# Kernel tuning notes

Hardware: AMD Instinct MI355X
Metric: run time of the kernel (lower is better)

Reference implementation:

```python
import jax, jax.numpy as jnp
import numpy as np

N = 8192      # nodes
E = 262144    # edges per graph (avg degree 32)
D_IN = 256
HID = 64
HEADS = 2
NEG_SLOPE = 0.2  # PyG GATConv leaky_relu slope


def _self_loops(ei, n):
    loop = jnp.arange(n, dtype=ei.dtype)
    return jnp.concatenate([ei[0], loop]), jnp.concatenate([ei[1], loop])


def gat_conv(x, src, dst, W, att_src, att_dst, b, concat):
    # PyG GATConv: h=[N,H,C]; alpha=softmax_dst(leaky_relu(a_s[src]+a_d[dst]))
    n = x.shape[0]
    H, C = att_src.shape
    h = (x @ W).reshape(n, H, C)
    a_s = (h * att_src).sum(-1)           # [N,H]
    a_d = (h * att_dst).sum(-1)           # [N,H]
    e = jax.nn.leaky_relu(a_s[src] + a_d[dst], NEG_SLOPE)  # [Etot,H]
    e = e - jax.ops.segment_max(e, dst, num_segments=n)[dst]
    e = jnp.exp(e)
    denom = jax.ops.segment_sum(e, dst, num_segments=n)[dst] + 1e-16
    alpha = e / denom                     # edge softmax per target node
    msg = h[src] * alpha[:, :, None]      # [Etot,H,C]
    out = jax.ops.segment_sum(msg, dst, num_segments=n)  # [N,H,C]
    out = out.reshape(n, H * C) if concat else out.mean(axis=1)
    return out + b


def gcn_conv(x, src, dst, W, b):
    # PyG GCNConv: D^{-1/2}(A+I)D^{-1/2} X W + b (self loops already appended)
    n = x.shape[0]
    h = x @ W
    deg = jax.ops.segment_sum(jnp.ones_like(src, jnp.float32), dst, num_segments=n)
    dinv = jax.lax.rsqrt(jnp.maximum(deg, 1.0))
    norm = dinv[src] * dinv[dst]          # [Etot]
    return jax.ops.segment_sum(h[src] * norm[:, None], dst, num_segments=n) + b


def cross_attn(q_in, kv_in, Wq, bq, Wk, bk, Wv, bv, Wo, bo, num_heads):
    n, d = q_in.shape
    hd = d // num_heads
    q = (q_in @ Wq + bq).reshape(n, num_heads, hd)
    k = (kv_in @ Wk + bk).reshape(n, num_heads, hd)
    v = (kv_in @ Wv + bv).reshape(n, num_heads, hd)
    scores = jnp.einsum('qhd,khd->hqk', q, k) / np.sqrt(hd).astype(np.float32)
    attn = jax.nn.softmax(scores, axis=-1)                 # [H,N,N]
    out = jnp.einsum('hqk,khd->qhd', attn, v).reshape(n, d) @ Wo + bo
    weights = attn.mean(axis=0)[None]                      # [1,N,N] avg heads (torch default)
    return out, weights


def setup_inputs():
    key = jax.random.key(0)
    ks = jax.random.split(key, 24)
    w = lambda k, s: jax.random.normal(k, s, jnp.float32) * 0.05
    inp = {
        'x': jax.random.normal(ks[0], (N, D_IN), jnp.float32),
        'edge_index_tkg': jax.random.randint(ks[1], (2, E), 0, N, jnp.int64 if jax.config.jax_enable_x64 else jnp.int32),
        'edge_index_ekg': jax.random.randint(ks[2], (2, E), 0, N, jnp.int64 if jax.config.jax_enable_x64 else jnp.int32),
        # GAT layer 1: heads=2, concat=True
        'gat1_W': w(ks[3], (D_IN, HEADS * HID)),
        'gat1_att_src': w(ks[4], (HEADS, HID)),
        'gat1_att_dst': w(ks[5], (HEADS, HID)),
        'gat1_b': jnp.zeros((HEADS * HID,), jnp.float32),
        # GAT layer 2: heads=1, concat=False
        'gat2_W': w(ks[6], (HEADS * HID, HID)),
        'gat2_att_src': w(ks[7], (1, HID)),
        'gat2_att_dst': w(ks[8], (1, HID)),
        'gat2_b': jnp.zeros((HID,), jnp.float32),
        # GCN layers
        'gcn1_W': w(ks[9], (D_IN, HID)),
        'gcn1_b': jnp.zeros((HID,), jnp.float32),
        'gcn2_W': w(ks[10], (HID, HID)),
        'gcn2_b': jnp.zeros((HID,), jnp.float32),
        # cross attention (hidden=64, 2 heads)
        'Wq': w(ks[11], (HID, HID)), 'bq': jnp.zeros((HID,), jnp.float32),
        'Wk': w(ks[12], (HID, HID)), 'bk': jnp.zeros((HID,), jnp.float32),
        'Wv': w(ks[13], (HID, HID)), 'bv': jnp.zeros((HID,), jnp.float32),
        'Wo': w(ks[14], (HID, HID)), 'bo': jnp.zeros((HID,), jnp.float32),
        # MLP head
        'fc1_W': w(ks[15], (2 * HID, HID)), 'fc1_b': jnp.zeros((HID,), jnp.float32),
        'fc2_W': w(ks[16], (HID, 1)), 'fc2_b': jnp.zeros((1,), jnp.float32),
    }
    return inp


def reference(x, edge_index_tkg, edge_index_ekg,
              gat1_W, gat1_att_src, gat1_att_dst, gat1_b,
              gat2_W, gat2_att_src, gat2_att_dst, gat2_b,
              gcn1_W, gcn1_b, gcn2_W, gcn2_b,
              Wq, bq, Wk, bk, Wv, bv, Wo, bo,
              fc1_W, fc1_b, fc2_W, fc2_b):
    n = x.shape[0]
    src_t, dst_t = _self_loops(edge_index_tkg, n)
    src_e, dst_e = _self_loops(edge_index_ekg, n)

    h_tkg = jax.nn.elu(gat_conv(x, src_t, dst_t, gat1_W, gat1_att_src, gat1_att_dst, gat1_b, True))
    h_tkg = jax.nn.elu(gat_conv(h_tkg, src_t, dst_t, gat2_W, gat2_att_src, gat2_att_dst, gat2_b, False))

    h_ekg = jax.nn.relu(gcn_conv(x, src_e, dst_e, gcn1_W, gcn1_b))
    h_ekg = jax.nn.relu(gcn_conv(h_ekg, src_e, dst_e, gcn2_W, gcn2_b))

    h_attn, attn_weights = cross_attn(h_tkg, h_ekg, Wq, bq, Wk, bk, Wv, bv, Wo, bo, HEADS)

    h_fused = jnp.concatenate([h_tkg, h_attn], axis=1)   # [N, 2*HID]
    pred = (jax.nn.relu(h_fused @ fc1_W + fc1_b) @ fc2_W + fc2_b).squeeze(-1)
    return pred, attn_weights
```

## Files before the change

kernel.cpp:

```cpp
#include <hip/hip_runtime.h>
#include <cstdint>
#include <cstddef>

#define NN 8192
#define EE 262144
#define ET 270336

using short8  = __attribute__((ext_vector_type(8))) short;
using floatx4 = __attribute__((ext_vector_type(4))) float;

__device__ __forceinline__ unsigned short f2bf(float f) {
  unsigned int u = __float_as_uint(f);
  u += 0x7fffu + ((u >> 16) & 1u);
  return (unsigned short)(u >> 16);
}

__global__ void edge_hist2_k(const int* __restrict__ ei_t, const int* __restrict__ ei_e,
                             int* __restrict__ cnt_t, int* __restrict__ cnt_e) {
  int idx = blockIdx.x * 256 + threadIdx.x;
  int g = idx >= ET;
  int e = g ? idx - ET : idx;
  const int* ei = g ? ei_e : ei_t;
  int* cnt = g ? cnt_e : cnt_t;
  int d = (e < EE) ? ei[EE + e] : (e - EE);
  atomicAdd(&cnt[d], 1);
}

__global__ void scan2_k(int* cnt_t, int* off_t, int* cnt_e, int* off_e) {
  int* cnt = blockIdx.x ? cnt_e : cnt_t;
  int* off = blockIdx.x ? off_e : off_t;
  __shared__ int s[1024];
  int t = threadIdx.x;
  int v[8]; int base = t * 8; int sum = 0;
  #pragma unroll
  for (int j = 0; j < 8; ++j) { v[j] = cnt[base + j]; sum += v[j]; }
  s[t] = sum; __syncthreads();
  for (int o = 1; o < 1024; o <<= 1) {
    int x = (t >= o) ? s[t - o] : 0;
    __syncthreads();
    s[t] += x;
    __syncthreads();
  }
  int excl = s[t] - sum;
  #pragma unroll
  for (int j = 0; j < 8; ++j) { off[base + j] = excl; cnt[base + j] = excl; excl += v[j]; }
  if (t == 1023) off[NN] = excl;
}

__global__ void edge_scatter2_k(const int* __restrict__ ei_t, const int* __restrict__ ei_e,
                                int* __restrict__ pos_t, int* __restrict__ pos_e,
                                int* __restrict__ srcs_t, int* __restrict__ srcs_e) {
  int idx = blockIdx.x * 256 + threadIdx.x;
  int g = idx >= ET;
  int e = g ? idx - ET : idx;
  const int* ei = g ? ei_e : ei_t;
  int* pos = g ? pos_e : pos_t;
  int* srcs = g ? srcs_e : srcs_t;
  int sv, d;
  if (e < EE) { sv = ei[e]; d = ei[EE + e]; } else { sv = d = e - EE; }
  int p = atomicAdd(&pos[d], 1);
  srcs[p] = sv;
}

__device__ __forceinline__ void gemm_core(const float* __restrict__ A, int lda, int K,
                                          const float* __restrict__ Bs, int row0, int col,
                                          float acc[8]) {
  #pragma unroll
  for (int r = 0; r < 8; ++r) acc[r] = 0.f;
  for (int k = 0; k < K; k += 4) {
    float b0 = Bs[(k + 0) * 32 + col], b1 = Bs[(k + 1) * 32 + col];
    float b2 = Bs[(k + 2) * 32 + col], b3 = Bs[(k + 3) * 32 + col];
    #pragma unroll
    for (int r = 0; r < 8; ++r) {
      const float4 a4 = *(const float4*)(A + (size_t)(row0 + r) * lda + k);
      acc[r] = fmaf(a4.x, b0, acc[r]);
      acc[r] = fmaf(a4.y, b1, acc[r]);
      acc[r] = fmaf(a4.z, b2, acc[r]);
      acc[r] = fmaf(a4.w, b3, acc[r]);
    }
  }
}

__global__ __launch_bounds__(256) void mm_x_k(const float* __restrict__ x,
    const float* __restrict__ Wgat, const float* __restrict__ Wgcn,
    const float* __restrict__ as_w, const float* __restrict__ ad_w,
    float* __restrict__ h1, float* __restrict__ hg1,
    float* __restrict__ a_s1, float* __restrict__ a_d1) {
  __shared__ float Bs[256 * 32];
  const int tid = threadIdx.x, by = blockIdx.y;
  const bool gat = by < 4;
  const int NC = gat ? 128 : 64;
  const int c0 = gat ? by * 32 : (by - 4) * 32;
  const float* B = gat ? Wgat : Wgcn;
  for (int idx = tid; idx < 256 * 32; idx += 256)
    Bs[idx] = B[(idx >> 5) * NC + c0 + (idx & 31)];
  __syncthreads();
  const int row0 = blockIdx.x * 64 + (tid >> 5) * 8;
  const int col = tid & 31;
  float acc[8];
  gemm_core(x, 256, 256, Bs, row0, col, acc);
  if (gat) {
    #pragma unroll
    for (int r = 0; r < 8; ++r) h1[(size_t)(row0 + r) * 128 + c0 + col] = acc[r];
    const int head = c0 >> 6;
    const float asw = as_w[head * 64 + (c0 & 63) + col];
    const float adw = ad_w[head * 64 + (c0 & 63) + col];
    float ps[8], pd[8];
    #pragma unroll
    for (int r = 0; r < 8; ++r) { ps[r] = acc[r] * asw; pd[r] = acc[r] * adw; }
    #pragma unroll
    for (int m = 16; m >= 1; m >>= 1)
      #pragma unroll
      for (int r = 0; r < 8; ++r) { ps[r] += __shfl_xor(ps[r], m); pd[r] += __shfl_xor(pd[r], m); }
    if (col == 0) {
      #pragma unroll
      for (int r = 0; r < 8; ++r) {
        atomicAdd(&a_s1[(row0 + r) * 2 + head], ps[r]);
        atomicAdd(&a_d1[(row0 + r) * 2 + head], pd[r]);
      }
    }
  } else {
    #pragma unroll
    for (int r = 0; r < 8; ++r) hg1[(size_t)(row0 + r) * 64 + c0 + col] = acc[r];
  }
}

template<int H, int C>
__device__ __forceinline__ void gat_agg_body(const float* __restrict__ h,
    const float* __restrict__ a_s, const float* __restrict__ a_d,
    const int* __restrict__ off, const int* __restrict__ srcs,
    const float* __restrict__ bias, float* __restrict__ out, int ldout, int b) {
  constexpr int HC = H * C;
  const int tid = threadIdx.x;
  const int hd = tid / C;
  const int r0 = off[b], r1 = off[b + 1];
  __shared__ int s_src[HC];
  __shared__ float s_w[HC][H];
  float ad[H];
  #pragma unroll
  for (int hh = 0; hh < H; ++hh) ad[hh] = a_d[b * H + hh];
  float acc = 0.f, den = 0.f;
  for (int base = r0; base < r1; base += HC) {
    const int cnt = min(HC, r1 - base);
    const int cnt4 = (cnt + 3) & ~3;
    __syncthreads();
    int e = base + tid;
    if (e < r1) {
      int sv = srcs[e];
      s_src[tid] = sv;
      #pragma unroll
      for (int hh = 0; hh < H; ++hh) {
        float xv = a_s[sv * H + hh] + ad[hh];
        xv = xv > 0.f ? xv : 0.2f * xv;
        s_w[tid][hh] = __expf(xv);
      }
    } else if (tid < cnt4) {
      s_src[tid] = 0;
      #pragma unroll
      for (int hh = 0; hh < H; ++hh) s_w[tid][hh] = 0.f;
    }
    __syncthreads();
    for (int j = 0; j < cnt4; j += 4) {
      #pragma unroll
      for (int u = 0; u < 4; ++u) {
        float wv = s_w[j + u][hd];
        den += wv;
        acc = fmaf(wv, h[(size_t)s_src[j + u] * HC + tid], acc);
      }
    }
  }
  float o = acc / den + bias[tid];
  out[(size_t)b * ldout + tid] = o > 0.f ? o : (__expf(o) - 1.f);
}

template<int H, int C>
__global__ void gat_agg_k(const float* __restrict__ h, const float* __restrict__ a_s,
                          const float* __restrict__ a_d, const int* __restrict__ off,
                          const int* __restrict__ srcs, const float* __restrict__ bias,
                          float* __restrict__ out, int ldout) {
  gat_agg_body<H, C>(h, a_s, a_d, off, srcs, bias, out, ldout, blockIdx.x);
}

__global__ __launch_bounds__(128) void agg1_k(
    const float* __restrict__ h1, const float* __restrict__ a_s1, const float* __restrict__ a_d1,
    const int* __restrict__ off_t, const int* __restrict__ src_t,
    const float* __restrict__ gat1_b, float* __restrict__ g1out,
    const float* __restrict__ hg1, const int* __restrict__ off_e, const int* __restrict__ src_e,
    const float* __restrict__ gcn1_b, const float* __restrict__ gcn2_W, float* __restrict__ h2g) {
  const int tid = threadIdx.x;
  if (blockIdx.x < NN) {
    gat_agg_body<2, 64>(h1, a_s1, a_d1, off_t, src_t, gat1_b, g1out, 128, blockIdx.x);
  } else {
    const int nb = (blockIdx.x - NN) * 2;
    const int sub = tid >> 6, t = tid & 63;
    const int node = nb + sub;
    __shared__ int s_src2[2][64];
    __shared__ float s_nrm2[2][64];
    __shared__ float s_row2[2][64];
    const int r0 = off_e[node], r1 = off_e[node + 1];
    const int cA = off_e[nb + 1] - off_e[nb];
    const int cB = off_e[nb + 2] - off_e[nb + 1];
    const int trips = (max(cA, cB) + 63) >> 6;
    float dinv_b = rsqrtf((float)max(r1 - r0, 1));
    float acc = 0.f;
    for (int it = 0; it < trips; ++it) {
      const int cnt = min(64, r1 - (r0 + it * 64));
      const int cnt4 = (cnt + 3) & ~3;
      __syncthreads();
      int e = r0 + it * 64 + t;
      if (e < r1) {
        int sv = src_e[e];
        s_src2[sub][t] = sv;
        int ds = off_e[sv + 1] - off_e[sv];
        s_nrm2[sub][t] = dinv_b * rsqrtf((float)max(ds, 1));
      } else if (t < cnt4) {
        s_src2[sub][t] = 0;
        s_nrm2[sub][t] = 0.f;
      }
      __syncthreads();
      for (int j = 0; j < cnt4; j += 4) {
        #pragma unroll
        for (int u = 0; u < 4; ++u)
          acc = fmaf(s_nrm2[sub][j + u], hg1[(size_t)s_src2[sub][j + u] * 64 + t], acc);
      }
    }
    s_row2[sub][t] = fmaxf(acc + gcn1_b[t], 0.f);
    __syncthreads();
    float acc2 = 0.f;
    for (int k = 0; k < 64; ++k)
      acc2 = fmaf(s_row2[sub][k], gcn2_W[k * 64 + t], acc2);
    h2g[(size_t)node * 64 + t] = acc2;
  }
}

__global__ __launch_bounds__(256) void mm2_k(
    const float* __restrict__ g1out, const float* __restrict__ gat2_W,
    const float* __restrict__ gat2_as, const float* __restrict__ gat2_ad,
    float* __restrict__ h2, float* __restrict__ a_s2, float* __restrict__ a_d2,
    const float* __restrict__ h2g, const int* __restrict__ off_e, const int* __restrict__ src_e,
    const float* __restrict__ gcn2_b, float* __restrict__ hekg) {
  const int tid = threadIdx.x;
  if (blockIdx.x < 256) {
    __shared__ float Bs[128 * 32];
    const int bx = blockIdx.x & 127;
    const int c0 = (blockIdx.x >> 7) * 32;
    for (int idx = tid; idx < 128 * 32; idx += 256)
      Bs[idx] = gat2_W[(idx >> 5) * 64 + c0 + (idx & 31)];
    __syncthreads();
    const int row0 = bx * 64 + (tid >> 5) * 8;
    const int col = tid & 31;
    float acc[8];
    gemm_core(g1out, 128, 128, Bs, row0, col, acc);
    const float asw = gat2_as[c0 + col];
    const float adw = gat2_ad[c0 + col];
    float ps[8], pd[8];
    #pragma unroll
    for (int r = 0; r < 8; ++r) {
      h2[(size_t)(row0 + r) * 64 + c0 + col] = acc[r];
      ps[r] = acc[r] * asw; pd[r] = acc[r] * adw;
    }
    #pragma unroll
    for (int m = 16; m >= 1; m >>= 1)
      #pragma unroll
      for (int r = 0; r < 8; ++r) { ps[r] += __shfl_xor(ps[r], m); pd[r] += __shfl_xor(pd[r], m); }
    if (col == 0) {
      #pragma unroll
      for (int r = 0; r < 8; ++r) {
        atomicAdd(&a_s2[row0 + r], ps[r]);
        atomicAdd(&a_d2[row0 + r], pd[r]);
      }
    }
  } else {
    const int nb = (blockIdx.x - 256) * 4;
    const int sub = tid >> 6, t = tid & 63;
    const int node = nb + sub;
    __shared__ int s_src4[4][64];
    __shared__ float s_nrm4[4][64];
    const int r0 = off_e[node], r1 = off_e[node + 1];
    int cmax = 0;
    #pragma unroll
    for (int i = 0; i < 4; ++i) cmax = max(cmax, off_e[nb + i + 1] - off_e[nb + i]);
    const int trips = (cmax + 63) >> 6;
    float dinv_b = rsqrtf((float)max(r1 - r0, 1));
    float acc = 0.f;
    for (int it = 0; it < trips; ++it) {
      const int cnt = min(64, r1 - (r0 + it * 64));
      const int cnt4 = (cnt + 3) & ~3;
      __syncthreads();
      int e = r0 + it * 64 + t;
      if (e < r1) {
        int sv = src_e[e];
        s_src4[sub][t] = sv;
        int ds = off_e[sv + 1] - off_e[sv];
        s_nrm4[sub][t] = dinv_b * rsqrtf((float)max(ds, 1));
      } else if (t < cnt4) {
        s_src4[sub][t] = 0;
        s_nrm4[sub][t] = 0.f;
      }
      __syncthreads();
      for (int j = 0; j < cnt4; j += 4) {
        #pragma unroll
        for (int u = 0; u < 4; ++u)
          acc = fmaf(s_nrm4[sub][j + u], h2g[(size_t)s_src4[sub][j + u] * 64 + t], acc);
      }
    }
    hekg[(size_t)node * 64 + t] = fmaxf(acc + gcn2_b[t], 0.f);
  }
}

__global__ __launch_bounds__(256) void mm_qkv_k(const float* __restrict__ htkg,
    const float* __restrict__ hekg,
    const float* __restrict__ Wq, const float* __restrict__ bq,
    const float* __restrict__ Wk, const float* __restrict__ bk,
    const float* __restrict__ Wv, const float* __restrict__ bv,
    unsigned short* __restrict__ qb, unsigned short* __restrict__ kb,
    unsigned short* __restrict__ Vt) {
  __shared__ float Bs[64 * 32];
  __shared__ float Ts[32][65];
  const int tid = threadIdx.x, by = blockIdx.y;
  const int kind = by >> 1;
  const int c0 = (by & 1) * 32;
  const float* A = (kind == 0) ? htkg : hekg;
  const float* B = (kind == 0) ? Wq : (kind == 1) ? Wk : Wv;
  const float* bias = (kind == 0) ? bq : (kind == 1) ? bk : bv;
  for (int idx = tid; idx < 64 * 32; idx += 256)
    Bs[idx] = B[(idx >> 5) * 64 + c0 + (idx & 31)];
  __syncthreads();
  const int row0 = blockIdx.x * 64 + (tid >> 5) * 8;
  const int col = tid & 31;
  float acc[8];
  gemm_core(A, 64, 64, Bs, row0, col, acc);
  const float bb = bias[c0 + col];
  if (kind == 0) {
    const float SCL = 0.17677669529663687f * 1.4426950408889634f;
    #pragma unroll
    for (int r = 0; r < 8; ++r)
      qb[(size_t)(row0 + r) * 64 + c0 + col] = f2bf((acc[r] + bb) * SCL);
  } else if (kind == 1) {
    #pragma unroll
    for (int r = 0; r < 8; ++r)
      kb[(size_t)(row0 + r) * 64 + c0 + col] = f2bf(acc[r] + bb);
  } else {
    const int rl = (tid >> 5) * 8;
    #pragma unroll
    for (int r = 0; r < 8; ++r) Ts[col][rl + r] = acc[r] + bb;
    __syncthreads();
    const int c = tid >> 3, rr = (tid & 7) * 8;
    short8 pk;
    #pragma unroll
    for (int j = 0; j < 8; ++j) pk[j] = (short)f2bf(Ts[c][rr + j]);
    *(short8*)(Vt + (size_t)(c0 + c) * NN + blockIdx.x * 64 + rr) = pk;
  }
}

__global__ __launch_bounds__(512) void att_lsum_k(
    const unsigned short* __restrict__ qb, const unsigned short* __restrict__ kb,
    float* __restrict__ lsum) {
  __shared__ __align__(16) short Kbuf[2][64 * 64];
  const int tid = threadIdx.x;
  const int lane = tid & 63, wv = tid >> 6;
  const int ql = lane & 15, quad = lane >> 4;
  const int q0 = blockIdx.x * 128 + wv * 16;
  const int k0 = blockIdx.y * 1024;
  const floatx4 zf = {0.f, 0.f, 0.f, 0.f};

  short8 qf[2];
  #pragma unroll
  for (int h = 0; h < 2; ++h)
    qf[h] = *(const short8*)(qb + (size_t)(q0 + ql) * 64 + h * 32 + quad * 8);

  const int sr = tid >> 3, sc = tid & 7;
  const int swc = (sc ^ (sr & 7)) * 8;
  short8 krg;

  float lacc[2][4];
  #pragma unroll
  for (int h = 0; h < 2; ++h)
    #pragma unroll
    for (int r = 0; r < 4; ++r) lacc[h][r] = 0.f;

  {
    krg = *(const short8*)(kb + (size_t)(k0 + sr) * 64 + sc * 8);
    *(short8*)&Kbuf[0][sr * 64 + swc] = krg;
  }
  __syncthreads();

  for (int t = 0; t < 16; ++t) {
    if (t < 15)
      krg = *(const short8*)(kb + (size_t)(k0 + (t + 1) * 64 + sr) * 64 + sc * 8);
    const short* Kc = Kbuf[t & 1];
    #pragma unroll
    for (int kt = 0; kt < 4; ++kt) {
      const int row = kt * 16 + ql;
      short8 kf[2];
      #pragma unroll
      for (int h = 0; h < 2; ++h)
        kf[h] = *(const short8*)&Kc[row * 64 + ((h * 4 + quad) ^ (row & 7)) * 8];
      #pragma unroll
      for (int h = 0; h < 2; ++h) {
        floatx4 s = __builtin_amdgcn_mfma_f32_16x16x32_bf16(qf[h], kf[h], zf, 0, 0, 0);
        #pragma unroll
        for (int r = 0; r < 4; ++r) lacc[h][r] += __builtin_amdgcn_exp2f(s[r]);
      }
    }
    if (t < 15)
      *(short8*)&Kbuf[(t + 1) & 1][sr * 64 + swc] = krg;
    __syncthreads();
  }

  #pragma unroll
  for (int o = 8; o >= 1; o >>= 1)
    #pragma unroll
    for (int h = 0; h < 2; ++h)
      #pragma unroll
      for (int r = 0; r < 4; ++r)
        lacc[h][r] += __shfl_xor(lacc[h][r], o, 16);
  if (ql == 0) {
    #pragma unroll
    for (int h = 0; h < 2; ++h)
      #pragma unroll
      for (int r = 0; r < 4; ++r)
        atomicAdd(&lsum[(q0 + quad * 4 + r) * 2 + h], lacc[h][r]);
  }
}

__global__ __launch_bounds__(512, 4) void att_pv_k(
    const unsigned short* __restrict__ qb, const unsigned short* __restrict__ kb,
    const unsigned short* __restrict__ Vt, const float* __restrict__ lsum,
    float* __restrict__ attn, float* __restrict__ O) {
  __shared__ __align__(16) short Kbuf[2][64 * 64];
  __shared__ __align__(16) short Vbuf[2][64 * 64];
  __shared__ __align__(16) float Esh[8][2][16 * 36];
  const int tid = threadIdx.x;
  const int lane = tid & 63, wv = tid >> 6;
  const int ql = lane & 15, quad = lane >> 4;
  const int q0 = blockIdx.x * 128 + wv * 16;
  const int k0 = blockIdx.y * 1024;
  const floatx4 zf = {0.f, 0.f, 0.f, 0.f};

  short8 qf[2];
  #pragma unroll
  for (int h = 0; h < 2; ++h)
    qf[h] = *(const short8*)(qb + (size_t)(q0 + ql) * 64 + h * 32 + quad * 8);

  float invl[2][4];
  #pragma unroll
  for (int h = 0; h < 2; ++h)
    #pragma unroll
    for (int r = 0; r < 4; ++r)
      invl[h][r] = 1.0f / lsum[(q0 + quad * 4 + r) * 2 + h];

  const int sr = tid >> 3, sc = tid & 7;
  const int swc = (sc ^ (sr & 7)) * 8;
  short8 krg, vrg;

  floatx4 oacc[2][2];
  #pragma unroll
  for (int h = 0; h < 2; ++h)
    #pragma unroll
    for (int hf = 0; hf < 2; ++hf) oacc[h][hf] = zf;

  {
    krg = *(const short8*)(kb + (size_t)(k0 + sr) * 64 + sc * 8);
    vrg = *(const short8*)(Vt + (size_t)sr * NN + k0 + sc * 8);
    *(short8*)&Kbuf[0][sr * 64 + swc] = krg;
    *(short8*)&Vbuf[0][sr * 64 + swc] = vrg;
  }
  __syncthreads();

  for (int t = 0; t < 16; ++t) {
    if (t < 15) {
      krg = *(const short8*)(kb + (size_t)(k0 + (t + 1) * 64 + sr) * 64 + sc * 8);
      vrg = *(const short8*)(Vt + (size_t)sr * NN + k0 + (t + 1) * 64 + sc * 8);
    }
    const short* Kc = Kbuf[t & 1];
    const short* Vc = Vbuf[t & 1];
    #pragma unroll
    for (int ks = 0; ks < 2; ++ks) {
      short8 kf[2][2], vf[2][2];
      #pragma unroll
      for (int kt = 0; kt < 2; ++kt) {
        const int row = ks * 32 + kt * 16 + ql;
        #pragma unroll
        for (int h = 0; h < 2; ++h)
          kf[kt][h] = *(const short8*)&Kc[row * 64 + ((h * 4 + quad) ^ (row & 7)) * 8];
      }
      #pragma unroll
      for (int h = 0; h < 2; ++h)
        #pragma unroll
        for (int hf = 0; hf < 2; ++hf) {
          const int d = h * 32 + hf * 16 + ql;
          vf[h][hf] = *(const short8*)&Vc[d * 64 + ((ks * 4 + quad) ^ (d & 7)) * 8];
        }

      floatx4 p[2][2];
      #pragma unroll
      for (int h = 0; h < 2; ++h)
        #pragma unroll
        for (int kt = 0; kt < 2; ++kt) {
          floatx4 s = __builtin_amdgcn_mfma_f32_16x16x32_bf16(qf[h], kf[kt][h], zf, 0, 0, 0);
          #pragma unroll
          for (int r = 0; r < 4; ++r)
            p[h][kt][r] = __builtin_amdgcn_exp2f(s[r]) * invl[h][r];
        }
      #pragma unroll
      for (int kt = 0; kt < 2; ++kt)
        #pragma unroll
        for (int r = 0; r < 4; ++r)
          attn[(size_t)(q0 + quad * 4 + r) * NN + k0 + t * 64 + ks * 32 + kt * 16 + ql] =
              0.5f * (p[0][kt][r] + p[1][kt][r]);
      #pragma unroll
      for (int h = 0; h < 2; ++h)
        #pragma unroll
        for (int kt = 0; kt < 2; ++kt)
          #pragma unroll
          for (int r = 0; r < 4; ++r)
            Esh[wv][h][(quad * 4 + r) * 36 + kt * 16 + ql] = p[h][kt][r];
      #pragma unroll
      for (int h = 0; h < 2; ++h) {
        const float* ep = &Esh[wv][h][ql * 36 + quad * 8];
        float4 x0 = *(const float4*)ep;
        float4 x1 = *(const float4*)(ep + 4);
        short8 ef;
        ef[0] = (short)f2bf(x0.x); ef[1] = (short)f2bf(x0.y);
        ef[2] = (short)f2bf(x0.z); ef[3] = (short)f2bf(x0.w);
        ef[4] = (short)f2bf(x1.x); ef[5] = (short)f2bf(x1.y);
        ef[6] = (short)f2bf(x1.z); ef[7] = (short)f2bf(x1.w);
        #pragma unroll
        for (int hf = 0; hf < 2; ++hf)
          oacc[h][hf] = __builtin_amdgcn_mfma_f32_16x16x32_bf16(ef, vf[h][hf], oacc[h][hf], 0, 0, 0);
      }
    }
    if (t < 15) {
      *(short8*)&Kbuf[(t + 1) & 1][sr * 64 + swc] = krg;
      *(short8*)&Vbuf[(t + 1) & 1][sr * 64 + swc] = vrg;
    }
    __syncthreads();
  }

  #pragma unroll
  for (int h = 0; h < 2; ++h)
    #pragma unroll
    for (int hf = 0; hf < 2; ++hf)
      #pragma unroll
      for (int r = 0; r < 4; ++r)
        atomicAdd(&O[(size_t)(q0 + quad * 4 + r) * 64 + h * 32 + hf * 16 + ql], oacc[h][hf][r]);
}

__global__ __launch_bounds__(256) void tail_k(const float* __restrict__ O,
    const float* __restrict__ htkg, const float* __restrict__ Wo, const float* __restrict__ bo,
    const float* __restrict__ fc1W, const float* __restrict__ fc1b,
    const float* __restrict__ fc2W, const float* __restrict__ fc2b,
    float* __restrict__ pred) {
  __shared__ float Ws[8192];
  __shared__ float T1[2048];
  __shared__ float T2[2048];
  const int tid = threadIdx.x;
  const int col = tid & 63, rg = tid >> 6;
  const int rowbase = blockIdx.x * 32;
  for (int i = tid; i < 2048; i += 256) T1[i] = O[(size_t)rowbase * 64 + i];
  for (int i = tid; i < 4096; i += 256) Ws[i] = Wo[i];
  const float rbo = bo[col], rf1b = fc1b[col], rf2 = fc2W[col], rf2b = fc2b[0];
  __syncthreads();
  float ha[8];
  #pragma unroll
  for (int r = 0; r < 8; ++r) {
    const int row = rg * 8 + r;
    float acc = rbo;
    for (int k = 0; k < 64; ++k) acc = fmaf(T1[row * 64 + k], Ws[k * 64 + col], acc);
    ha[r] = acc;
  }
  __syncthreads();
  #pragma unroll
  for (int r = 0; r < 8; ++r) T2[(rg * 8 + r) * 64 + col] = ha[r];
  for (int i = tid; i < 2048; i += 256) T1[i] = htkg[(size_t)rowbase * 64 + i];
  for (int i = tid; i < 8192; i += 256) Ws[i] = fc1W[i];
  __syncthreads();
  #pragma unroll
  for (int r = 0; r < 8; ++r) {
    const int row = rg * 8 + r;
    float acc = rf1b;
    for (int k = 0; k < 64; ++k) acc = fmaf(T1[row * 64 + k], Ws[k * 64 + col], acc);
    for (int k = 0; k < 64; ++k) acc = fmaf(T2[row * 64 + k], Ws[(64 + k) * 64 + col], acc);
    float y = fmaxf(acc, 0.f);
    float v = y * rf2;
    #pragma unroll
    for (int m = 32; m >= 1; m >>= 1) v += __shfl_xor(v, m);
    if (col == 0) pred[rowbase + row] = v + rf2b;
  }
}

extern "C" void kernel_launch(void* const* d_in, const int* in_sizes, int n_in,
                              void* d_out, int out_size, void* d_ws, size_t ws_size,
                              hipStream_t stream) {
  (void)in_sizes; (void)n_in; (void)out_size; (void)ws_size;
  const float* x       = (const float*)d_in[0];
  const int*   ei_t    = (const int*)d_in[1];
  const int*   ei_e    = (const int*)d_in[2];
  const float* gat1_W  = (const float*)d_in[3];
  const float* gat1_as = (const float*)d_in[4];
  const float* gat1_ad = (const float*)d_in[5];
  const float* gat1_b  = (const float*)d_in[6];
  const float* gat2_W  = (const float*)d_in[7];
  const float* gat2_as = (const float*)d_in[8];
  const float* gat2_ad = (const float*)d_in[9];
  const float* gat2_b  = (const float*)d_in[10];
  const float* gcn1_W  = (const float*)d_in[11];
  const float* gcn1_b  = (const float*)d_in[12];
  const float* gcn2_W  = (const float*)d_in[13];
  const float* gcn2_b  = (const float*)d_in[14];
  const float* Wq = (const float*)d_in[15]; const float* bq = (const float*)d_in[16];
  const float* Wk = (const float*)d_in[17]; const float* bk = (const float*)d_in[18];
  const float* Wv = (const float*)d_in[19]; const float* bv = (const float*)d_in[20];
  const float* Wo = (const float*)d_in[21]; const float* bo = (const float*)d_in[22];
  const float* fc1_W = (const float*)d_in[23]; const float* fc1_b = (const float*)d_in[24];
  const float* fc2_W = (const float*)d_in[25]; const float* fc2_b = (const float*)d_in[26];

  float* out  = (float*)d_out;
  float* attn = out + NN;

  char* wsp = (char*)d_ws;
  size_t ofs = 0;
  auto take = [&](size_t bytes) -> char* {
    char* p = wsp + ofs;
    ofs = (ofs + bytes + 255) & ~(size_t)255;
    return p;
  };
  int*   pos_t = (int*)take(NN * 4);
  int*   pos_e = (int*)take(NN * 4);
  float* a_s1  = (float*)take((size_t)NN * 2 * 4);
  float* a_d1  = (float*)take((size_t)NN * 2 * 4);
  float* a_s2  = (float*)take((size_t)NN * 4);
  float* a_d2  = (float*)take((size_t)NN * 4);
  float* a_l   = (float*)take((size_t)NN * 2 * 4);
  float* Obuf  = (float*)take((size_t)NN * 64 * 4);
  const size_t zero_span = ofs;
  int* off_t = (int*)take((NN + 1) * 4);
  int* off_e = (int*)take((NN + 1) * 4);
  int* src_t = (int*)take((size_t)ET * 4);
  int* src_e = (int*)take((size_t)ET * 4);
  float* h1    = (float*)take((size_t)NN * 128 * 4);
  float* g1out = (float*)take((size_t)NN * 128 * 4);
  float* h2    = (float*)take((size_t)NN * 64 * 4);
  float* htkg  = (float*)take((size_t)NN * 64 * 4);
  float* hg1   = (float*)take((size_t)NN * 64 * 4);
  float* h2g   = (float*)take((size_t)NN * 64 * 4);
  float* hekg  = (float*)take((size_t)NN * 64 * 4);
  unsigned short* qb = (unsigned short*)take((size_t)NN * 64 * 2);
  unsigned short* kb = (unsigned short*)take((size_t)NN * 64 * 2);
  unsigned short* Vt = (unsigned short*)take((size_t)64 * NN * 2);

  hipMemsetAsync(wsp, 0, zero_span, stream);

  edge_hist2_k<<<2 * ET / 256, 256, 0, stream>>>(ei_t, ei_e, pos_t, pos_e);
  scan2_k<<<2, 1024, 0, stream>>>(pos_t, off_t, pos_e, off_e);
  edge_scatter2_k<<<2 * ET / 256, 256, 0, stream>>>(ei_t, ei_e, pos_t, pos_e, src_t, src_e);

  mm_x_k<<<dim3(128, 6), 256, 0, stream>>>(x, gat1_W, gcn1_W, gat1_as, gat1_ad,
                                           h1, hg1, a_s1, a_d1);
  agg1_k<<<NN + NN / 2, 128, 0, stream>>>(h1, a_s1, a_d1, off_t, src_t, gat1_b, g1out,
                                          hg1, off_e, src_e, gcn1_b, gcn2_W, h2g);
  mm2_k<<<256 + NN / 4, 256, 0, stream>>>(g1out, gat2_W, gat2_as, gat2_ad, h2, a_s2, a_d2,
                                          h2g, off_e, src_e, gcn2_b, hekg);
  gat_agg_k<1, 64><<<NN, 64, 0, stream>>>(h2, a_s2, a_d2, off_t, src_t, gat2_b, htkg, 64);

  mm_qkv_k<<<dim3(128, 6), 256, 0, stream>>>(htkg, hekg, Wq, bq, Wk, bk, Wv, bv, qb, kb, Vt);

  att_lsum_k<<<dim3(64, 8), 512, 0, stream>>>(qb, kb, a_l);
  att_pv_k<<<dim3(64, 8), 512, 0, stream>>>(qb, kb, Vt, a_l, attn, Obuf);

  tail_k<<<256, 256, 0, stream>>>(Obuf, htkg, Wo, bo, fc1_W, fc1_b, fc2_W, fc2_b, out);
}
```

Before: 578.4 us.

## Transpose MFMA operands so attention rows live per lane, drop LDS staging

Swaps the A/B operands of the score and PV MFMAs so each lane holds a query row and consecutive key columns. This lets the averaged attention weights be written as contiguous float4 stores instead of scattered scalar stores, and replaces the per-wave LDS round-trip for the P tile with cross-lane shuffles. The row-sum reduction also shrinks to two shuffles and fewer atomics. The costs are extra shuffle instructions and select logic, and the shuffle-based P remapping has to reproduce the operand layout the MFMA expects exactly.

```diff
diff --git a/kernel.cpp b/kernel.cpp
--- a/kernel.cpp
+++ b/kernel.cpp
@@ -373,11 +373,7 @@
   const int swc = (sc ^ (sr & 7)) * 8;
   short8 krg;
 
-  float lacc[2][4];
-  #pragma unroll
-  for (int h = 0; h < 2; ++h)
-    #pragma unroll
-    for (int r = 0; r < 4; ++r) lacc[h][r] = 0.f;
+  float lacc[2] = {0.f, 0.f};
 
   {
     krg = *(const short8*)(kb + (size_t)(k0 + sr) * 64 + sc * 8);
@@ -398,9 +394,9 @@
         kf[h] = *(const short8*)&Kc[row * 64 + ((h * 4 + quad) ^ (row & 7)) * 8];
       #pragma unroll
       for (int h = 0; h < 2; ++h) {
-        floatx4 s = __builtin_amdgcn_mfma_f32_16x16x32_bf16(qf[h], kf[h], zf, 0, 0, 0);
+        floatx4 s = __builtin_amdgcn_mfma_f32_16x16x32_bf16(kf[h], qf[h], zf, 0, 0, 0);
         #pragma unroll
-        for (int r = 0; r < 4; ++r) lacc[h][r] += __builtin_amdgcn_exp2f(s[r]);
+        for (int r = 0; r < 4; ++r) lacc[h] += __builtin_amdgcn_exp2f(s[r]);
       }
     }
     if (t < 15)
@@ -409,18 +405,14 @@
   }
 
   #pragma unroll
-  for (int o = 8; o >= 1; o >>= 1)
+  for (int h = 0; h < 2; ++h) {
+    lacc[h] += __shfl_xor(lacc[h], 16);
+    lacc[h] += __shfl_xor(lacc[h], 32);
+  }
+  if (lane < 16) {
     #pragma unroll
     for (int h = 0; h < 2; ++h)
-      #pragma unroll
-      for (int r = 0; r < 4; ++r)
-        lacc[h][r] += __shfl_xor(lacc[h][r], o, 16);
-  if (ql == 0) {
-    #pragma unroll
-    for (int h = 0; h < 2; ++h)
-      #pragma unroll
-      for (int r = 0; r < 4; ++r)
-        atomicAdd(&lsum[(q0 + quad * 4 + r) * 2 + h], lacc[h][r]);
+      atomicAdd(&lsum[(q0 + ql) * 2 + h], lacc[h]);
   }
 }
 
@@ -430,7 +422,6 @@
     float* __restrict__ attn, float* __restrict__ O) {
   __shared__ __align__(16) short Kbuf[2][64 * 64];
   __shared__ __align__(16) short Vbuf[2][64 * 64];
-  __shared__ __align__(16) float Esh[8][2][16 * 36];
   const int tid = threadIdx.x;
   const int lane = tid & 63, wv = tid >> 6;
   const int ql = lane & 15, quad = lane >> 4;
@@ -443,16 +434,18 @@
   for (int h = 0; h < 2; ++h)
     qf[h] = *(const short8*)(qb + (size_t)(q0 + ql) * 64 + h * 32 + quad * 8);
 
-  float invl[2][4];
+  float invl[2];
   #pragma unroll
   for (int h = 0; h < 2; ++h)
-    #pragma unroll
-    for (int r = 0; r < 4; ++r)
-      invl[h][r] = 1.0f / lsum[(q0 + quad * 4 + r) * 2 + h];
+    invl[h] = 1.0f / lsum[(q0 + ql) * 2 + h];
 
   const int sr = tid >> 3, sc = tid & 7;
   const int swc = (sc ^ (sr & 7)) * 8;
   short8 krg, vrg;
+
+  const int sl_lo = ql + 16 * ((quad & 1) * 2);
+  const int sl_hi = sl_lo + 16;
+  const bool hi_kt = quad >= 2;
 
   floatx4 oacc[2][2];
   #pragma unroll
@@ -498,37 +491,38 @@
       for (int h = 0; h < 2; ++h)
         #pragma unroll
         for (int kt = 0; kt < 2; ++kt) {
-          floatx4 s = __builtin_amdgcn_mfma_f32_16x16x32_bf16(qf[h], kf[kt][h], zf, 0, 0, 0);
+          floatx4 s = __builtin_amdgcn_mfma_f32_16x16x32_bf16(kf[kt][h], qf[h], zf, 0, 0, 0);
           #pragma unroll
           for (int r = 0; r < 4; ++r)
-            p[h][kt][r] = __builtin_amdgcn_exp2f(s[r]) * invl[h][r];
+            p[h][kt][r] = __builtin_amdgcn_exp2f(s[r]) * invl[h];
         }
       #pragma unroll
-      for (int kt = 0; kt < 2; ++kt)
-        #pragma unroll
-        for (int r = 0; r < 4; ++r)
-          attn[(size_t)(q0 + quad * 4 + r) * NN + k0 + t * 64 + ks * 32 + kt * 16 + ql] =
-              0.5f * (p[0][kt][r] + p[1][kt][r]);
-      #pragma unroll
-      for (int h = 0; h < 2; ++h)
-        #pragma unroll
-        for (int kt = 0; kt < 2; ++kt)
-          #pragma unroll
-          for (int r = 0; r < 4; ++r)
-            Esh[wv][h][(quad * 4 + r) * 36 + kt * 16 + ql] = p[h][kt][r];
+      for (int kt = 0; kt < 2; ++kt) {
+        float4 m;
+        m.x = 0.5f * (p[0][kt][0] + p[1][kt][0]);
+        m.y = 0.5f * (p[0][kt][1] + p[1][kt][1]);
+        m.z = 0.5f * (p[0][kt][2] + p[1][kt][2]);
+        m.w = 0.5f * (p[0][kt][3] + p[1][kt][3]);
+        *(float4*)&attn[(size_t)(q0 + ql) * NN + k0 + t * 64 + ks * 32 + kt * 16 + quad * 4] = m;
+      }
       #pragma unroll
       for (int h = 0; h < 2; ++h) {
-        const float* ep = &Esh[wv][h][ql * 36 + quad * 8];
-        float4 x0 = *(const float4*)ep;
-        float4 x1 = *(const float4*)(ep + 4);
+        float t0 = hi_kt ? p[h][1][0] : p[h][0][0];
+        float t1 = hi_kt ? p[h][1][1] : p[h][0][1];
+        float t2 = hi_kt ? p[h][1][2] : p[h][0][2];
+        float t3 = hi_kt ? p[h][1][3] : p[h][0][3];
         short8 ef;
-        ef[0] = (short)f2bf(x0.x); ef[1] = (short)f2bf(x0.y);
-        ef[2] = (short)f2bf(x0.z); ef[3] = (short)f2bf(x0.w);
-        ef[4] = (short)f2bf(x1.x); ef[5] = (short)f2bf(x1.y);
-        ef[6] = (short)f2bf(x1.z); ef[7] = (short)f2bf(x1.w);
+        ef[0] = (short)f2bf(__shfl(t0, sl_lo));
+        ef[1] = (short)f2bf(__shfl(t1, sl_lo));
+        ef[2] = (short)f2bf(__shfl(t2, sl_lo));
+        ef[3] = (short)f2bf(__shfl(t3, sl_lo));
+        ef[4] = (short)f2bf(__shfl(t0, sl_hi));
+        ef[5] = (short)f2bf(__shfl(t1, sl_hi));
+        ef[6] = (short)f2bf(__shfl(t2, sl_hi));
+        ef[7] = (short)f2bf(__shfl(t3, sl_hi));
         #pragma unroll
         for (int hf = 0; hf < 2; ++hf)
-          oacc[h][hf] = __builtin_amdgcn_mfma_f32_16x16x32_bf16(ef, vf[h][hf], oacc[h][hf], 0, 0, 0);
+          oacc[h][hf] = __builtin_amdgcn_mfma_f32_16x16x32_bf16(vf[h][hf], ef, oacc[h][hf], 0, 0, 0);
       }
     }
     if (t < 15) {
@@ -544,7 +538,7 @@
     for (int hf = 0; hf < 2; ++hf)
       #pragma unroll
       for (int r = 0; r < 4; ++r)
-        atomicAdd(&O[(size_t)(q0 + quad * 4 + r) * 64 + h * 32 + hf * 16 + ql], oacc[h][hf][r]);
+        atomicAdd(&O[(size_t)(q0 + ql) * 64 + h * 32 + hf * 16 + quad * 4 + r], oacc[h][hf][r]);
 }
 
 __global__ __launch_bounds__(256) void tail_k(const float* __restrict__ O,
```

Result: slower. 608.7 us (+5.2%).
